# Performance work log

Hardware: AMD Instinct MI355X
Metric: run time of the kernel (lower is better)

Reference implementation:

```python
import jax, jax.numpy as jnp
import numpy as np

INV_SQRT2 = 0.7071067811865476
EPS = 1e-6


def _ln(x, w, b):
    m = x.mean(-1, keepdims=True)
    v = ((x - m) ** 2).mean(-1, keepdims=True)
    return (x - m) * jax.lax.rsqrt(v + 1e-5) * w + b


def setup_inputs() -> dict:
    key = jax.random.key(0)
    ks = jax.random.split(key, 18)
    B, L, D, H = 4, 2048, 1024, 16
    Dh = D // H
    Nf = L // 2 + 1
    s = 0.02
    inp = {
        "x": jax.random.normal(ks[0], (B, L, D), jnp.float32),
        "Wq": jax.random.normal(ks[1], (D, D), jnp.float32) * s,
        "Wv": jax.random.normal(ks[2], (D, D), jnp.float32) * s,
        "Wo": jax.random.normal(ks[3], (D, D), jnp.float32) * s,
        # gate MLP: LayerNorm(Dh) -> Linear(Dh,4Dh) -> GELU -> Linear(4Dh, 2*Nf)
        "g_ln_w": jnp.ones((Dh,), jnp.float32),
        "g_ln_b": jnp.zeros((Dh,), jnp.float32),
        "g_w1": jax.random.normal(ks[4], (Dh, 4 * Dh), jnp.float32) * s,
        "g_b1": jnp.zeros((4 * Dh,), jnp.float32),
        "g_w2": jax.random.normal(ks[5], (4 * Dh, 2 * Nf), jnp.float32) * s,
        "g_b2": jnp.zeros((2 * Nf,), jnp.float32),
        # shared modReLU bias (1, Nf)
        "mod_bias": jax.random.normal(ks[6], (1, Nf), jnp.float32) * s,
        # wavelet gating MLP: LayerNorm(Dh) -> Linear(Dh,Dh) -> GELU -> Linear(Dh,Dh) -> Sigmoid
        "w_ln_w": jnp.ones((Dh,), jnp.float32),
        "w_ln_b": jnp.zeros((Dh,), jnp.float32),
        "w_w1": jax.random.normal(ks[7], (Dh, Dh), jnp.float32) * s,
        "w_b1": jnp.zeros((Dh,), jnp.float32),
        "w_w2": jax.random.normal(ks[8], (Dh, Dh), jnp.float32) * s,
        "w_b2": jnp.zeros((Dh,), jnp.float32),
    }
    return inp


def _spectre_forward(x, Wq, Wv, Wo, g_ln_w, g_ln_b, g_w1, g_b1, g_w2, g_b2,
                     mod_bias, w_ln_w, w_ln_b, w_w1, w_b1, w_w2, w_b2):
    B, L, D = x.shape
    H = 16
    Dh = D // H
    Nf = L // 2 + 1

    q = (x @ Wq).reshape(B, L, H, Dh).transpose(0, 2, 1, 3)  # (B,H,L,Dh)
    v = (x @ Wv).reshape(B, L, H, Dh).transpose(0, 2, 1, 3)  # (B,H,L,Dh)

    q_mean = q.mean(axis=2)  # (B,H,Dh) global query summary

    # spectral gates from global query
    h = _ln(q_mean, g_ln_w, g_ln_b)
    h = jax.nn.gelu(h @ g_w1 + g_b1, approximate=False)
    gate = h @ g_w2 + g_b2  # (B,H,2*Nf)
    g = jax.lax.complex(gate[..., :Nf], gate[..., Nf:])  # (B,H,Nf)

    # complex modReLU on the gate (toeplitz_bandwidth = 0 -> identity)
    mag = jnp.abs(g)
    g = (jax.nn.relu(mag + mod_bias) / (mag + EPS)).astype(g.dtype) * g

    # frequency-domain mixing of v
    Vf = jnp.fft.rfft(v, axis=2)  # (B,H,Nf,Dh)
    Vf = Vf * g[..., None]
    v_mix = jnp.fft.irfft(Vf, n=L, axis=2).astype(x.dtype)  # (B,H,L,Dh)

    # wavelet refinement (eval mode: never skipped)
    # single-level depthwise Haar along L
    a = jnp.asarray(INV_SQRT2, x.dtype)
    ev, od = v_mix[:, :, 0::2, :], v_mix[:, :, 1::2, :]  # (B,H,L/2,Dh)
    lp = (ev + od) * a
    hp = (od - ev) * a

    wh = _ln(q_mean, w_ln_w, w_ln_b)
    wh = jax.nn.gelu(wh @ w_w1 + w_b1, approximate=False)
    wgate = jax.nn.sigmoid(wh @ w_w2 + w_b2)  # (B,H,Dh)
    lp = lp * wgate[:, :, None, :]
    hp = hp * wgate[:, :, None, :]

    # Haar synthesis (perfect reconstruction when gate == 1)
    rec_ev = (lp - hp) * a
    rec_od = (lp + hp) * a
    recon = jnp.stack([rec_ev, rec_od], axis=3).reshape(B, H, L, Dh)
    v_mix = v_mix + recon

    out = v_mix.transpose(0, 2, 1, 3).reshape(B, L, D) @ Wo
    return out


def reference(x, Wq, Wv, Wo, g_ln_w, g_ln_b, g_w1, g_b1, g_w2, g_b2,
              mod_bias, w_ln_w, w_ln_b, w_w1, w_b1, w_w2, w_b2):
    return _spectre_forward(x, Wq, Wv, Wo, g_ln_w, g_ln_b, g_w1, g_b1, g_w2,
                            g_b2, mod_bias, w_ln_w, w_ln_b, w_w1, w_b1, w_w2,
                            w_b2)
```

## Files before the change

### kernel.cpp

```cpp
#include <hip/hip_runtime.h>
#include <hip/hip_fp16.h>
#include <math.h>

typedef unsigned short u16;
typedef _Float16 f16x8 __attribute__((ext_vector_type(8)));
typedef float f32x4 __attribute__((ext_vector_type(4)));
typedef u16 u16x8 __attribute__((ext_vector_type(8)));

#define B_ 4
#define L_ 2048
#define D_ 1024
#define H_ 16
#define DH 64
#define NF 1025
#define BH (B_*H_)

#define Z_OFF    0
#define G_OFF    8388608
#define WSC_OFF  (G_OFF + 262144)
#define XB_OFF   (WSC_OFF + 4096)
#define PART_OFF (XB_OFF + 4096)
#define H1_OFF   (PART_OFF + 131072)
#define QP_OFF   (H1_OFF + 16384)
#define XHI_OFF  (QP_OFF + 32768)
#define WVH_OFF  (XHI_OFF + 4194304)
#define WOH_OFF  (WVH_OFF + 524288)

__device__ __forceinline__ u16 f2h(float f) {
    __half h = __float2half(f);
    return *reinterpret_cast<u16*>(&h);
}

__global__ void k_xbar1(const float* __restrict__ x, float* __restrict__ part) {
    int t = threadIdx.x;
    int dblk = blockIdx.x, lc = blockIdx.y, b = blockIdx.z;
    int d = dblk*256 + t;
    const float* px = x + ((size_t)b*L_ + (size_t)lc*64)*D_ + d;
    float s = 0.f;
    #pragma unroll 4
    for (int l = 0; l < 64; ++l) s += px[(size_t)l*D_];
    part[(size_t)(b*32 + lc)*D_ + d] = s;
}

__global__ void k_xbar2(const float* __restrict__ part, float* __restrict__ xbar) {
    int id = blockIdx.x*256 + threadIdx.x;
    int b = id >> 10, d = id & 1023;
    float s = 0.f;
    for (int c = 0; c < 32; ++c) s += part[(size_t)(b*32 + c)*D_ + d];
    xbar[id] = s * (1.0f/(float)L_);
}

__global__ void k_qmean1(const float* __restrict__ xbar, const float* __restrict__ Wq,
                         float* __restrict__ qpart) {
    int t = threadIdx.x;
    int dblk = blockIdx.x, b = blockIdx.y, kc = blockIdx.z;
    int d = dblk*256 + t;
    const float* xb = xbar + b*D_ + kc*128;
    const float* wq = Wq + (size_t)(kc*128)*D_ + d;
    float s = 0.f;
    #pragma unroll 8
    for (int k = 0; k < 128; ++k) s += xb[k] * wq[(size_t)k*D_];
    qpart[((size_t)kc*B_ + b)*D_ + d] = s;
}

__global__ void k_gates_a(const float* __restrict__ qpart,
                          const float* __restrict__ g_ln_w, const float* __restrict__ g_ln_b,
                          const float* __restrict__ g_w1,  const float* __restrict__ g_b1,
                          const float* __restrict__ w_ln_w, const float* __restrict__ w_ln_b,
                          const float* __restrict__ w_w1,  const float* __restrict__ w_b1,
                          const float* __restrict__ w_w2,  const float* __restrict__ w_b2,
                          float* __restrict__ h1_out, float* __restrict__ wscale) {
    int bh = blockIdx.x;
    int b = bh >> 4, h = bh & 15;
    int t = threadIdx.x;
    __shared__ float qm[64], hg[64], wh[64], w1o[64];

    if (t < 64) {
        float s = 0.f;
        #pragma unroll
        for (int kc = 0; kc < 8; ++kc)
            s += qpart[((size_t)kc*B_ + b)*D_ + h*64 + t];
        qm[t] = s;
    }
    __syncthreads();

    float m = 0.f;
    #pragma unroll
    for (int k = 0; k < 64; ++k) m += qm[k];
    m *= (1.0f/64.0f);
    float var = 0.f;
    #pragma unroll
    for (int k = 0; k < 64; ++k) { float df = qm[k]-m; var += df*df; }
    var *= (1.0f/64.0f);
    float rs = rsqrtf(var + 1e-5f);
    if (t < 64) {
        float c = (qm[t]-m)*rs;
        hg[t] = c*g_ln_w[t] + g_ln_b[t];
        wh[t] = c*w_ln_w[t] + w_ln_b[t];
    }
    __syncthreads();

    {
        float acc = g_b1[t];
        #pragma unroll 16
        for (int k = 0; k < 64; ++k) acc += hg[k]*g_w1[k*256 + t];
        h1_out[bh*256 + t] = 0.5f*acc*(1.0f + erff(acc*0.70710678118654752f));
    }
    if (t < 64) {
        float acc = w_b1[t];
        #pragma unroll 16
        for (int k = 0; k < 64; ++k) acc += wh[k]*w_w1[k*64 + t];
        w1o[t] = 0.5f*acc*(1.0f + erff(acc*0.70710678118654752f));
    }
    __syncthreads();

    if (t < 64) {
        float acc = w_b2[t];
        #pragma unroll 16
        for (int k = 0; k < 64; ++k) acc += w1o[k]*w_w2[k*64 + t];
        wscale[bh*64 + t] = 1.0f + 1.0f/(1.0f + expf(-acc));
    }
}

__global__ __launch_bounds__(256) void k_gate_g(const float* __restrict__ h1_ws,
                                                const float* __restrict__ g_w2,
                                                const float* __restrict__ g_b2,
                                                const float* __restrict__ mod_bias,
                                                float* __restrict__ G) {
    int bh = blockIdx.y;
    int t = threadIdx.x;
    int w = t >> 6, l = t & 63;
    int f = blockIdx.x*64 + l;
    int fc = f < NF ? f : NF-1;
    __shared__ float h1s[256];
    __shared__ float rre[4][64], rim[4][64];
    h1s[t] = h1_ws[bh*256 + t];
    __syncthreads();

    float re = 0.f, im = 0.f;
    const float* gw = g_w2 + (size_t)(w*64)*2050;
    const float* h1p = h1s + w*64;
    #pragma unroll 8
    for (int k = 0; k < 64; ++k) {
        float hv = h1p[k];
        re += hv * gw[(size_t)k*2050 + fc];
        im += hv * gw[(size_t)k*2050 + NF + fc];
    }
    rre[w][l] = re; rim[w][l] = im;
    __syncthreads();
    if (w == 0 && f < NF) {
        float rr = rre[0][l]+rre[1][l]+rre[2][l]+rre[3][l] + g_b2[f];
        float ii = rim[0][l]+rim[1][l]+rim[2][l]+rim[3][l] + g_b2[NF+f];
        float mag = sqrtf(rr*rr + ii*ii);
        float mult = fmaxf(mag + mod_bias[f], 0.f) / (mag + 1e-6f);
        float s = mult * (1.0f/2048.0f);
        float gr = s*rr, gi = s*ii;
        if (f == 0 || f == 1024) gi = 0.f;
        float* Gb = G + (size_t)bh*4096;
        Gb[2*f]   = gr;
        Gb[2*f+1] = gi;
        if (f >= 1 && f <= 1023) {
            Gb[2*(2048-f)]   = gr;
            Gb[2*(2048-f)+1] = -gi;
        }
    }
}

__global__ void k_xhalf(const float4* __restrict__ x, u16* __restrict__ hi) {
    int i = blockIdx.x*256 + threadIdx.x;
    float4 v = x[i];
    ushort4 h;
    h.x = f2h(v.x);
    h.y = f2h(v.y);
    h.z = f2h(v.z);
    h.w = f2h(v.w);
    ((ushort4*)hi)[i] = h;
}

__global__ void k_wsplit(const float* __restrict__ Wv, const float* __restrict__ Wo,
                         u16* __restrict__ WvH, u16* __restrict__ WoH) {
    const float* W = blockIdx.z ? Wo : Wv;
    u16* TH = blockIdx.z ? WoH : WvH;
    __shared__ float tile[32][33];
    int t = threadIdx.x;
    int n0 = blockIdx.x*32, k0 = blockIdx.y*32;
    #pragma unroll
    for (int i = 0; i < 4; ++i) {
        int k = (t >> 5) + 8*i;
        tile[k][t & 31] = W[(size_t)(k0 + k)*D_ + n0 + (t & 31)];
    }
    __syncthreads();
    int n = t >> 3, kc = (t & 7)*4;
    ushort4 h;
    h.x = f2h(tile[kc+0][n]);
    h.y = f2h(tile[kc+1][n]);
    h.z = f2h(tile[kc+2][n]);
    h.w = f2h(tile[kc+3][n]);
    *(ushort4*)&TH[(size_t)(n0 + n)*D_ + k0 + kc] = h;
}

template<int EPI>
__global__ __launch_bounds__(256) void k_mfma_gemm(const u16* __restrict__ Ahi,
                                                   const u16* __restrict__ Bhi,
                                                   float* __restrict__ C) {
    __shared__ u16 AsH[64*64], BsH[128*64];
    int t = threadIdx.x;
    size_t rowBase = (size_t)blockIdx.x * 64;
    int colBase = blockIdx.y * 128;
    f32x4 acc[2][4] = {};
    int lane = t & 63;
    int wr = (t >> 7) & 1, wc = (t >> 6) & 1;
    int lr = lane & 15, lq = lane >> 4;

    for (int k0 = 0; k0 < 1024; k0 += 64) {
        #pragma unroll
        for (int i = 0; i < 2; ++i) {
            int c = t + i*256;
            int r = c >> 3, cs = c & 7;
            int ko = (cs ^ (r & 7)) << 3;
            __builtin_amdgcn_global_load_lds(
                (const __attribute__((address_space(1))) void*)(Ahi + (rowBase + (size_t)r)*D_ + k0 + ko),
                (__attribute__((address_space(3))) void*)(AsH + c*8), 16, 0, 0);
        }
        #pragma unroll
        for (int i = 0; i < 4; ++i) {
            int c = t + i*256;
            int r = c >> 3, cs = c & 7;
            int ko = (cs ^ (r & 7)) << 3;
            __builtin_amdgcn_global_load_lds(
                (const __attribute__((address_space(1))) void*)(Bhi + ((size_t)colBase + r)*D_ + k0 + ko),
                (__attribute__((address_space(3))) void*)(BsH + c*8), 16, 0, 0);
        }
        __syncthreads();
        #pragma unroll
        for (int ks = 0; ks < 2; ++ks) {
            f16x8 ah[2], bh[4];
            #pragma unroll
            for (int m = 0; m < 2; ++m) {
                int row = wr*32 + m*16 + lr;
                int ch = (ks*4 + lq) ^ (row & 7);
                ah[m] = *(const f16x8*)(AsH + row*64 + ch*8);
            }
            #pragma unroll
            for (int n = 0; n < 4; ++n) {
                int row = wc*64 + n*16 + lr;
                int ch = (ks*4 + lq) ^ (row & 7);
                bh[n] = *(const f16x8*)(BsH + row*64 + ch*8);
            }
            #pragma unroll
            for (int m = 0; m < 2; ++m) {
                #pragma unroll
                for (int n = 0; n < 4; ++n) {
                    acc[m][n] = __builtin_amdgcn_mfma_f32_16x16x32_f16(ah[m], bh[n], acc[m][n], 0, 0, 0);
                }
            }
        }
        __syncthreads();
    }

    int cr = lq * 4, cc = lane & 15;
    if (EPI == 0) {
        #pragma unroll
        for (int m = 0; m < 2; ++m) {
            #pragma unroll
            for (int n = 0; n < 4; ++n) {
                int d = colBase + wc*64 + n*16 + cc;
                int hh = d >> 6, pr = (d >> 1) & 31, p = d & 1;
                #pragma unroll
                for (int r = 0; r < 4; ++r) {
                    size_t gr = rowBase + wr*32 + m*16 + cr + r;
                    int b = (int)(gr >> 11), l = (int)(gr & 2047);
                    C[(((size_t)((b*16 + hh)*32 + pr))*L_ + l)*2 + p] = acc[m][n][r];
                }
            }
        }
    } else {
        #pragma unroll
        for (int m = 0; m < 2; ++m) {
            #pragma unroll
            for (int n = 0; n < 4; ++n) {
                int d = colBase + wc*64 + n*16 + cc;
                #pragma unroll
                for (int r = 0; r < 4; ++r) {
                    size_t gr = rowBase + wr*32 + m*16 + cr + r;
                    C[gr*D_ + d] = acc[m][n][r];
                }
            }
        }
    }
}

__device__ __forceinline__ float2 cmulp(float2 a, float2 b) {
    return make_float2(a.x*b.x - a.y*b.y, a.x*b.y + a.y*b.x);
}
__device__ __forceinline__ float2 cadd(float2 a, float2 b){ return make_float2(a.x+b.x, a.y+b.y); }
__device__ __forceinline__ float2 csub(float2 a, float2 b){ return make_float2(a.x-b.x, a.y-b.y); }
__device__ __forceinline__ float2 cnegi(float2 a){ return make_float2(a.y, -a.x); }
__device__ __forceinline__ float2 cposi(float2 a){ return make_float2(-a.y, a.x); }

#define RH_ 0.70710678118654752f

__device__ __forceinline__ void fwd3(float2* e, float2 w1) {
    float2 tA1 = make_float2((w1.x + w1.y)*RH_, (w1.y - w1.x)*RH_);
    float2 tA2 = cnegi(w1);
    float2 tA3 = make_float2((w1.y - w1.x)*RH_, -(w1.x + w1.y)*RH_);
    float2 a, b, d;
    a=e[0]; b=e[4]; e[0]=cadd(a,b); d=csub(a,b); e[4]=cmulp(d, w1);
    a=e[1]; b=e[5]; e[1]=cadd(a,b); d=csub(a,b); e[5]=cmulp(d, tA1);
    a=e[2]; b=e[6]; e[2]=cadd(a,b); d=csub(a,b); e[6]=cmulp(d, tA2);
    a=e[3]; b=e[7]; e[3]=cadd(a,b); d=csub(a,b); e[7]=cmulp(d, tA3);
    float2 w2 = cmulp(w1,w1); float2 w2n = cnegi(w2);
    a=e[0]; b=e[2]; e[0]=cadd(a,b); d=csub(a,b); e[2]=cmulp(d, w2);
    a=e[1]; b=e[3]; e[1]=cadd(a,b); d=csub(a,b); e[3]=cmulp(d, w2n);
    a=e[4]; b=e[6]; e[4]=cadd(a,b); d=csub(a,b); e[6]=cmulp(d, w2);
    a=e[5]; b=e[7]; e[5]=cadd(a,b); d=csub(a,b); e[7]=cmulp(d, w2n);
    float2 w4 = cmulp(w2,w2);
    a=e[0]; b=e[1]; e[0]=cadd(a,b); d=csub(a,b); e[1]=cmulp(d, w4);
    a=e[2]; b=e[3]; e[2]=cadd(a,b); d=csub(a,b); e[3]=cmulp(d, w4);
    a=e[4]; b=e[5]; e[4]=cadd(a,b); d=csub(a,b); e[5]=cmulp(d, w4);
    a=e[6]; b=e[7]; e[6]=cadd(a,b); d=csub(a,b); e[7]=cmulp(d, w4);
}

__device__ __forceinline__ void inv3(float2* e, float2 b1) {
    float2 b2 = cmulp(b1,b1), b4 = cmulp(b2,b2);
    float2 a, bb;
    bb=cmulp(e[1],b4); a=e[0]; e[0]=cadd(a,bb); e[1]=csub(a,bb);
    bb=cmulp(e[3],b4); a=e[2]; e[2]=cadd(a,bb); e[3]=csub(a,bb);
    bb=cmulp(e[5],b4); a=e[4]; e[4]=cadd(a,bb); e[5]=csub(a,bb);
    bb=cmulp(e[7],b4); a=e[6]; e[6]=cadd(a,bb); e[7]=csub(a,bb);
    float2 b2i = cposi(b2);
    bb=cmulp(e[2],b2);  a=e[0]; e[0]=cadd(a,bb); e[2]=csub(a,bb);
    bb=cmulp(e[3],b2i); a=e[1]; e[1]=cadd(a,bb); e[3]=csub(a,bb);
    bb=cmulp(e[6],b2);  a=e[4]; e[4]=cadd(a,bb); e[6]=csub(a,bb);
    bb=cmulp(e[7],b2i); a=e[5]; e[5]=cadd(a,bb); e[7]=csub(a,bb);
    float2 tB1 = make_float2((b1.x - b1.y)*RH_, (b1.x + b1.y)*RH_);
    float2 tB2 = cposi(b1);
    float2 tB3 = make_float2(-(b1.x + b1.y)*RH_, (b1.x - b1.y)*RH_);
    bb=cmulp(e[4],b1);  a=e[0]; e[0]=cadd(a,bb); e[4]=csub(a,bb);
    bb=cmulp(e[5],tB1); a=e[1]; e[1]=cadd(a,bb); e[5]=csub(a,bb);
    bb=cmulp(e[6],tB2); a=e[2]; e[2]=cadd(a,bb); e[6]=csub(a,bb);
    bb=cmulp(e[7],tB3); a=e[3]; e[3]=cadd(a,bb); e[7]=csub(a,bb);
}

__device__ __forceinline__ void inv2(float2* e, float2 b1) {
    float2 b2 = cmulp(b1,b1);
    float2 a, bb;
    bb=cmulp(e[1],b2); a=e[0]; e[0]=cadd(a,bb); e[1]=csub(a,bb);
    bb=cmulp(e[3],b2); a=e[2]; e[2]=cadd(a,bb); e[3]=csub(a,bb);
    float2 b1i = cposi(b1);
    bb=cmulp(e[2],b1);  a=e[0]; e[0]=cadd(a,bb); e[2]=csub(a,bb);
    bb=cmulp(e[3],b1i); a=e[1]; e[1]=cadd(a,bb); e[3]=csub(a,bb);
}

#define PIDX(i) ((i) + ((i)>>5))

__global__ __launch_bounds__(256, 4) void k_fft(float* __restrict__ z,
                                                const float* __restrict__ G,
                                                const float* __restrict__ wscale) {
    __shared__ float2 dsh[2112];
    int t = threadIdx.x;
    int row = blockIdx.x;
    int bh = row >> 5, jp = row & 31;
    float2* zr = (float2*)z + (size_t)row * L_;
    const float PIO = 3.14159265358979323846f;

    float2 e[8];
    #pragma unroll
    for (int j = 0; j < 8; ++j) e[j] = zr[t + 256*j];
    {
        float s_, c_; __sincosf(-(PIO/1024.f)*(float)t, &s_, &c_);
        fwd3(e, make_float2(c_, s_));
    }
    #pragma unroll
    for (int j = 0; j < 8; ++j) { int i = t + 256*j; dsh[PIDX(i)] = e[j]; }
    __syncthreads();

    {
        int q = t >> 5, r = t & 31, base = q*256 + r;
        #pragma unroll
        for (int j = 0; j < 8; ++j) { int i = base + 32*j; e[j] = dsh[PIDX(i)]; }
        float s_, c_; __sincosf(-(PIO/128.f)*(float)r, &s_, &c_);
        fwd3(e, make_float2(c_, s_));
        #pragma unroll
        for (int j = 0; j < 8; ++j) { int i = base + 32*j; dsh[PIDX(i)] = e[j]; }
    }
    __syncthreads();

    {
        int q = t >> 2, r = t & 3, base = q*32 + r;
        #pragma unroll
        for (int j = 0; j < 8; ++j) { int i = base + 4*j; e[j] = dsh[PIDX(i)]; }
        float s_, c_; __sincosf(-(PIO/16.f)*(float)r, &s_, &c_);
        fwd3(e, make_float2(c_, s_));
        #pragma unroll
        for (int j = 0; j < 8; ++j) { int i = base + 4*j; dsh[PIDX(i)] = e[j]; }
    }
    __syncthreads();

    {
        #pragma unroll
        for (int u = 0; u < 8; ++u) { int i = 8*t + u; e[u] = dsh[PIDX(i)]; }
        float2 a, b, d;
        a=e[0]; b=e[2]; e[0]=cadd(a,b); e[2]=csub(a,b);
        a=e[1]; b=e[3]; e[1]=cadd(a,b); d=csub(a,b); e[3]=cnegi(d);
        a=e[4]; b=e[6]; e[4]=cadd(a,b); e[6]=csub(a,b);
        a=e[5]; b=e[7]; e[5]=cadd(a,b); d=csub(a,b); e[7]=cnegi(d);
        a=e[0]; b=e[1]; e[0]=cadd(a,b); e[1]=csub(a,b);
        a=e[2]; b=e[3]; e[2]=cadd(a,b); e[3]=csub(a,b);
        a=e[4]; b=e[5]; e[4]=cadd(a,b); e[5]=csub(a,b);
        a=e[6]; b=e[7]; e[6]=cadd(a,b); e[7]=csub(a,b);
        int flo = (int)(__brev((unsigned)t) >> 24);
        const float2* Gb = (const float2*)(G + (size_t)bh*4096);
        e[0] = cmulp(e[0], Gb[flo + 256*0]);
        e[1] = cmulp(e[1], Gb[flo + 256*4]);
        e[2] = cmulp(e[2], Gb[flo + 256*2]);
        e[3] = cmulp(e[3], Gb[flo + 256*6]);
        e[4] = cmulp(e[4], Gb[flo + 256*1]);
        e[5] = cmulp(e[5], Gb[flo + 256*5]);
        e[6] = cmulp(e[6], Gb[flo + 256*3]);
        e[7] = cmulp(e[7], Gb[flo + 256*7]);
        inv3(e, make_float2(1.f, 0.f));
        #pragma unroll
        for (int u = 0; u < 8; ++u) { int i = 8*t + u; dsh[PIDX(i)] = e[u]; }
    }
    __syncthreads();

    {
        int q = t >> 3, r = t & 7, base = q*64 + r;
        #pragma unroll
        for (int j = 0; j < 8; ++j) { int i = base + 8*j; e[j] = dsh[PIDX(i)]; }
        float s_, c_; __sincosf((PIO/32.f)*(float)r, &s_, &c_);
        inv3(e, make_float2(c_, s_));
        #pragma unroll
        for (int j = 0; j < 8; ++j) { int i = base + 8*j; dsh[PIDX(i)] = e[j]; }
    }
    __syncthreads();

    {
        int q = t >> 6, r = t & 63, base = q*512 + r;
        #pragma unroll
        for (int j = 0; j < 8; ++j) { int i = base + 64*j; e[j] = dsh[PIDX(i)]; }
        float s_, c_; __sincosf((PIO/256.f)*(float)r, &s_, &c_);
        inv3(e, make_float2(c_, s_));
        #pragma unroll
        for (int j = 0; j < 8; ++j) { int i = base + 64*j; dsh[PIDX(i)] = e[j]; }
    }
    __syncthreads();

    {
        #pragma unroll
        for (int j = 0; j < 4; ++j) { int i = t + 512*j; e[j] = dsh[PIDX(i)]; }
        #pragma unroll
        for (int j = 0; j < 4; ++j) { int i = t + 256 + 512*j; e[4+j] = dsh[PIDX(i)]; }
        float s_, c_; __sincosf((PIO/1024.f)*(float)t, &s_, &c_);
        float2 b1 = make_float2(c_, s_);
        inv2(e, b1);
        float2 b1b = make_float2((b1.x - b1.y)*RH_, (b1.x + b1.y)*RH_);
        inv2(e+4, b1b);
        float sc0 = wscale[bh*64 + 2*jp];
        float sc1 = wscale[bh*64 + 2*jp + 1];
        #pragma unroll
        for (int j = 0; j < 4; ++j) zr[t + 512*j] = make_float2(e[j].x*sc0, e[j].y*sc1);
        #pragma unroll
        for (int j = 0; j < 4; ++j) zr[t + 256 + 512*j] = make_float2(e[4+j].x*sc0, e[4+j].y*sc1);
    }
}

__global__ void k_vsplit(const float* __restrict__ z, u16* __restrict__ vhi) {
    int t = threadIdx.x;
    int lt = blockIdx.x, h = blockIdx.y, b = blockIdx.z;
    int l0 = lt*64;
    __shared__ float tile[64][65];
    const float2* zb = (const float2*)z + (size_t)(b*16 + h)*32*L_;
    int pr = t >> 3, lg = t & 7;
    #pragma unroll
    for (int i = 0; i < 8; ++i) {
        int l = lg*8 + i;
        float2 v = zb[(size_t)pr*L_ + l0 + l];
        tile[l][2*pr]   = v.x;
        tile[l][2*pr+1] = v.y;
    }
    __syncthreads();
    int l = t >> 2, d0 = (t & 3) * 16;
    u16x8 h0, h1v;
    #pragma unroll
    for (int i = 0; i < 8; ++i) h0[i]  = f2h(tile[l][d0+i]);
    #pragma unroll
    for (int i = 0; i < 8; ++i) h1v[i] = f2h(tile[l][d0+8+i]);
    size_t base = ((size_t)(b*L_) + l0 + l)*D_ + h*64 + d0;
    *(u16x8*)&vhi[base]   = h0;
    *(u16x8*)&vhi[base+8] = h1v;
}

extern "C" void kernel_launch(void* const* d_in, const int* in_sizes, int n_in,
                              void* d_out, int out_size, void* d_ws, size_t ws_size,
                              hipStream_t stream) {
    const float* x      = (const float*)d_in[0];
    const float* Wq     = (const float*)d_in[1];
    const float* Wv     = (const float*)d_in[2];
    const float* Wo     = (const float*)d_in[3];
    const float* g_ln_w = (const float*)d_in[4];
    const float* g_ln_b = (const float*)d_in[5];
    const float* g_w1   = (const float*)d_in[6];
    const float* g_b1   = (const float*)d_in[7];
    const float* g_w2   = (const float*)d_in[8];
    const float* g_b2   = (const float*)d_in[9];
    const float* mod_b  = (const float*)d_in[10];
    const float* w_ln_w = (const float*)d_in[11];
    const float* w_ln_b = (const float*)d_in[12];
    const float* w_w1   = (const float*)d_in[13];
    const float* w_b1   = (const float*)d_in[14];
    const float* w_w2   = (const float*)d_in[15];
    const float* w_b2   = (const float*)d_in[16];

    float* ws   = (float*)d_ws;
    float* z    = ws + Z_OFF;
    float* G    = ws + G_OFF;
    float* wsc  = ws + WSC_OFF;
    float* xbar = ws + XB_OFF;
    float* part = ws + PART_OFF;
    float* h1ws = ws + H1_OFF;
    float* qpart= ws + QP_OFF;
    u16* xhi = (u16*)(ws + XHI_OFF);
    u16* WvH = (u16*)(ws + WVH_OFF);
    u16* WoH = (u16*)(ws + WOH_OFF);
    u16* vhi = xhi;
    float* outp = (float*)d_out;

    dim3 gx(4, 32, 4);
    k_xbar1<<<gx, 256, 0, stream>>>(x, part);
    k_xbar2<<<16, 256, 0, stream>>>(part, xbar);
    dim3 gq(4, 4, 8);
    k_qmean1<<<gq, 256, 0, stream>>>(xbar, Wq, qpart);
    k_gates_a<<<64, 256, 0, stream>>>(qpart, g_ln_w, g_ln_b, g_w1, g_b1,
                                      w_ln_w, w_ln_b, w_w1, w_b1, w_w2, w_b2,
                                      h1ws, wsc);
    dim3 ggate(17, 64);
    k_gate_g<<<ggate, 256, 0, stream>>>(h1ws, g_w2, g_b2, mod_b, G);
    k_xhalf<<<8192, 256, 0, stream>>>((const float4*)x, xhi);
    dim3 gw(32, 32, 2);
    k_wsplit<<<gw, 256, 0, stream>>>(Wv, Wo, WvH, WoH);

    dim3 gg(128, 8);
    k_mfma_gemm<0><<<gg, 256, 0, stream>>>(xhi, WvH, z);
    k_fft<<<2048, 256, 0, stream>>>(z, G, wsc);
    dim3 gv(32, 16, 4);
    k_vsplit<<<gv, 256, 0, stream>>>(z, vhi);
    k_mfma_gemm<1><<<gg, 256, 0, stream>>>(vhi, WoH, outp);
}
```

Baseline: 141.7 us.

## Store FFT intermediate in fp16 and fuse x half conversion into mean pass

The V-projection GEMM now writes its output as packed fp16 pairs instead of fp32. The FFT kernel and the transpose kernel read and write this half-precision buffer, which halves their intermediate memory traffic and lets the transpose skip its conversion step. Separately, the fp16 copy of x is now produced inside the column-sum kernel, so the standalone conversion kernel is gone and x is read once fewer. Storing FFT inputs and outputs in fp16 risks extra rounding error on the spectral path.

```diff
diff --git a/kernel.cpp b/kernel.cpp
--- a/kernel.cpp
+++ b/kernel.cpp
@@ -16,7 +16,7 @@
 #define BH (B_*H_)
 
 #define Z_OFF    0
-#define G_OFF    8388608
+#define G_OFF    4194304
 #define WSC_OFF  (G_OFF + 262144)
 #define XB_OFF   (WSC_OFF + 4096)
 #define PART_OFF (XB_OFF + 4096)
@@ -30,15 +30,27 @@
     __half h = __float2half(f);
     return *reinterpret_cast<u16*>(&h);
 }
-
-__global__ void k_xbar1(const float* __restrict__ x, float* __restrict__ part) {
+__device__ __forceinline__ float h2fu(unsigned u) {
+    u16 v = (u16)u;
+    __half h = *reinterpret_cast<__half*>(&v);
+    return __half2float(h);
+}
+
+__global__ void k_xbar1h(const float* __restrict__ x, float* __restrict__ part,
+                         u16* __restrict__ xhi) {
     int t = threadIdx.x;
     int dblk = blockIdx.x, lc = blockIdx.y, b = blockIdx.z;
     int d = dblk*256 + t;
-    const float* px = x + ((size_t)b*L_ + (size_t)lc*64)*D_ + d;
+    size_t rowbase = (size_t)b*L_ + (size_t)lc*64;
+    const float* px = x + rowbase*D_ + d;
+    u16* ph = xhi + rowbase*D_ + d;
     float s = 0.f;
     #pragma unroll 4
-    for (int l = 0; l < 64; ++l) s += px[(size_t)l*D_];
+    for (int l = 0; l < 64; ++l) {
+        float v = px[(size_t)l*D_];
+        s += v;
+        ph[(size_t)l*D_] = f2h(v);
+    }
     part[(size_t)(b*32 + lc)*D_ + d] = s;
 }
 
@@ -164,17 +176,6 @@
             Gb[2*(2048-f)+1] = -gi;
         }
     }
-}
-
-__global__ void k_xhalf(const float4* __restrict__ x, u16* __restrict__ hi) {
-    int i = blockIdx.x*256 + threadIdx.x;
-    float4 v = x[i];
-    ushort4 h;
-    h.x = f2h(v.x);
-    h.y = f2h(v.y);
-    h.z = f2h(v.z);
-    h.w = f2h(v.w);
-    ((ushort4*)hi)[i] = h;
 }
 
 __global__ void k_wsplit(const float* __restrict__ Wv, const float* __restrict__ Wo,
@@ -260,6 +261,7 @@
 
     int cr = lq * 4, cc = lane & 15;
     if (EPI == 0) {
+        u16* Z = (u16*)C;
         #pragma unroll
         for (int m = 0; m < 2; ++m) {
             #pragma unroll
@@ -270,7 +272,7 @@
                 for (int r = 0; r < 4; ++r) {
                     size_t gr = rowBase + wr*32 + m*16 + cr + r;
                     int b = (int)(gr >> 11), l = (int)(gr & 2047);
-                    C[(((size_t)((b*16 + hh)*32 + pr))*L_ + l)*2 + p] = acc[m][n][r];
+                    Z[(((size_t)((b*16 + hh)*32 + pr))*L_ + l)*2 + p] = f2h(acc[m][n][r]);
                 }
             }
         }
@@ -354,19 +356,22 @@
 
 #define PIDX(i) ((i) + ((i)>>5))
 
-__global__ __launch_bounds__(256, 4) void k_fft(float* __restrict__ z,
+__global__ __launch_bounds__(256, 4) void k_fft(unsigned* __restrict__ z16,
                                                 const float* __restrict__ G,
                                                 const float* __restrict__ wscale) {
     __shared__ float2 dsh[2112];
     int t = threadIdx.x;
     int row = blockIdx.x;
     int bh = row >> 5, jp = row & 31;
-    float2* zr = (float2*)z + (size_t)row * L_;
+    unsigned* zr = z16 + (size_t)row * L_;
     const float PIO = 3.14159265358979323846f;
 
     float2 e[8];
     #pragma unroll
-    for (int j = 0; j < 8; ++j) e[j] = zr[t + 256*j];
+    for (int j = 0; j < 8; ++j) {
+        unsigned u = zr[t + 256*j];
+        e[j] = make_float2(h2fu(u & 0xffffu), h2fu(u >> 16));
+    }
     {
         float s_, c_; __sincosf(-(PIO/1024.f)*(float)t, &s_, &c_);
         fwd3(e, make_float2(c_, s_));
@@ -460,36 +465,48 @@
         float sc0 = wscale[bh*64 + 2*jp];
         float sc1 = wscale[bh*64 + 2*jp + 1];
         #pragma unroll
-        for (int j = 0; j < 4; ++j) zr[t + 512*j] = make_float2(e[j].x*sc0, e[j].y*sc1);
-        #pragma unroll
-        for (int j = 0; j < 4; ++j) zr[t + 256 + 512*j] = make_float2(e[4+j].x*sc0, e[4+j].y*sc1);
-    }
-}
-
-__global__ void k_vsplit(const float* __restrict__ z, u16* __restrict__ vhi) {
+        for (int j = 0; j < 4; ++j) {
+            unsigned lo = f2h(e[j].x*sc0), hi = f2h(e[j].y*sc1);
+            zr[t + 512*j] = lo | (hi << 16);
+        }
+        #pragma unroll
+        for (int j = 0; j < 4; ++j) {
+            unsigned lo = f2h(e[4+j].x*sc0), hi = f2h(e[4+j].y*sc1);
+            zr[t + 256 + 512*j] = lo | (hi << 16);
+        }
+    }
+}
+
+__global__ void k_vsplit(const unsigned* __restrict__ z16, u16* __restrict__ vhi) {
     int t = threadIdx.x;
     int lt = blockIdx.x, h = blockIdx.y, b = blockIdx.z;
     int l0 = lt*64;
-    __shared__ float tile[64][65];
-    const float2* zb = (const float2*)z + (size_t)(b*16 + h)*32*L_;
+    __shared__ unsigned tile[64][33];
+    const unsigned* zb = z16 + (size_t)(b*16 + h)*32*L_;
     int pr = t >> 3, lg = t & 7;
     #pragma unroll
     for (int i = 0; i < 8; ++i) {
         int l = lg*8 + i;
-        float2 v = zb[(size_t)pr*L_ + l0 + l];
-        tile[l][2*pr]   = v.x;
-        tile[l][2*pr+1] = v.y;
-    }
-    __syncthreads();
-    int l = t >> 2, d0 = (t & 3) * 16;
-    u16x8 h0, h1v;
-    #pragma unroll
-    for (int i = 0; i < 8; ++i) h0[i]  = f2h(tile[l][d0+i]);
-    #pragma unroll
-    for (int i = 0; i < 8; ++i) h1v[i] = f2h(tile[l][d0+8+i]);
-    size_t base = ((size_t)(b*L_) + l0 + l)*D_ + h*64 + d0;
-    *(u16x8*)&vhi[base]   = h0;
-    *(u16x8*)&vhi[base+8] = h1v;
+        tile[l][pr] = zb[(size_t)pr*L_ + l0 + l];
+    }
+    __syncthreads();
+    int l = t >> 2, q0 = (t & 3) * 8;
+    u16x8 o0, o1;
+    #pragma unroll
+    for (int i = 0; i < 4; ++i) {
+        unsigned u = tile[l][q0+i];
+        o0[2*i]   = (u16)(u & 0xffffu);
+        o0[2*i+1] = (u16)(u >> 16);
+    }
+    #pragma unroll
+    for (int i = 0; i < 4; ++i) {
+        unsigned u = tile[l][q0+4+i];
+        o1[2*i]   = (u16)(u & 0xffffu);
+        o1[2*i+1] = (u16)(u >> 16);
+    }
+    size_t base = ((size_t)(b*L_) + l0 + l)*D_ + h*64 + q0*2;
+    *(u16x8*)&vhi[base]   = o0;
+    *(u16x8*)&vhi[base+8] = o1;
 }
 
 extern "C" void kernel_launch(void* const* d_in, const int* in_sizes, int n_in,
@@ -514,7 +531,7 @@
     const float* w_b2   = (const float*)d_in[16];
 
     float* ws   = (float*)d_ws;
-    float* z    = ws + Z_OFF;
+    unsigned* z16 = (unsigned*)(ws + Z_OFF);
     float* G    = ws + G_OFF;
     float* wsc  = ws + WSC_OFF;
     float* xbar = ws + XB_OFF;
@@ -528,7 +545,7 @@
     float* outp = (float*)d_out;
 
     dim3 gx(4, 32, 4);
-    k_xbar1<<<gx, 256, 0, stream>>>(x, part);
+    k_xbar1h<<<gx, 256, 0, stream>>>(x, part, xhi);
     k_xbar2<<<16, 256, 0, stream>>>(part, xbar);
     dim3 gq(4, 4, 8);
     k_qmean1<<<gq, 256, 0, stream>>>(xbar, Wq, qpart);
@@ -537,14 +554,13 @@
                                       h1ws, wsc);
     dim3 ggate(17, 64);
     k_gate_g<<<ggate, 256, 0, stream>>>(h1ws, g_w2, g_b2, mod_b, G);
-    k_xhalf<<<8192, 256, 0, stream>>>((const float4*)x, xhi);
     dim3 gw(32, 32, 2);
     k_wsplit<<<gw, 256, 0, stream>>>(Wv, Wo, WvH, WoH);
 
     dim3 gg(128, 8);
-    k_mfma_gemm<0><<<gg, 256, 0, stream>>>(xhi, WvH, z);
-    k_fft<<<2048, 256, 0, stream>>>(z, G, wsc);
+    k_mfma_gemm<0><<<gg, 256, 0, stream>>>(xhi, WvH, (float*)z16);
+    k_fft<<<2048, 256, 0, stream>>>(z16, G, wsc);
     dim3 gv(32, 16, 4);
-    k_vsplit<<<gv, 256, 0, stream>>>(z, vhi);
+    k_vsplit<<<gv, 256, 0, stream>>>(z16, vhi);
     k_mfma_gemm<1><<<gg, 256, 0, stream>>>(vhi, WoH, outp);
 }
```

Measured after the change: 131.7 us, median of 2. -7.0%, faster.
